# Performance work log

Hardware: AMD Instinct MI355X
Metric: run time of the kernel (lower is better)

## Reference

```python
import jax, jax.numpy as jnp
import numpy as np

BATCH, SEQ, DIN, FILTERS, KSIZE = 64, 512, 256, 256, 3

def setup_inputs() -> dict:
    key = jax.random.key(0)
    ks = jax.random.split(key, 5)
    s_u = 1.0 / np.sqrt(DIN)
    return {
        "x": jax.random.normal(ks[0], (BATCH, SEQ, DIN), dtype=jnp.float32),
        "z": jax.random.normal(ks[1], (BATCH, DIN), dtype=jnp.float32),
        "U": jax.random.normal(ks[2], (DIN, DIN), dtype=jnp.float32) * s_u,
        "V": jax.random.normal(ks[3], (DIN, KSIZE * FILTERS), dtype=jnp.float32) * s_u,
        "B_w": jax.random.normal(ks[4], (DIN, KSIZE * FILTERS), dtype=jnp.float32) * s_u,
        "b": jnp.zeros((FILTERS,), dtype=jnp.float32),
        "kernel_size": KSIZE,
    }

def reference(x, z, U, V, B_w, b, kernel_size):
    Bn, L, din = x.shape
    K = int(kernel_size)
    F = V.shape[1] // K
    # per-sample dynamic kernel: (U * sigmoid(z)) @ V + B
    zf = jax.nn.sigmoid(z)                                  # (B, din)
    f = jnp.einsum('de,be,ef->bdf', U, zf, V) + B_w[None]    # (B, din, K*F)
    f = f.reshape(Bn, din, K, F).transpose(0, 2, 1, 3)       # (B, K, din, F)
    # 'same' padding, stride 1
    pad_l, pad_r = (K - 1) // 2, K // 2
    xp = jnp.pad(x, ((0, 0), (pad_l, pad_r), (0, 0)))        # (B, L+K-1, din)
    patches = jnp.stack([xp[:, i:i + L] for i in range(K)], axis=2)  # (B, L, K, din)
    out = jnp.einsum('blkd,bkdf->blf', patches, f) + b       # (B, L, F)
    return jax.nn.relu(out)
```

## Files before the change

kernel.cpp:

```cpp
#include <hip/hip_runtime.h>
#include <math.h>

#define BATCH 64
#define SEQL  512
#define DIN   256
#define NF    256
#define KS    3
#define KF    (KS * NF)

#define XCH 512
#define KC  (KS * XCH)
#define PROWS 130
#define PLD   128
#define PSZ   (PROWS * PLD)

typedef __attribute__((ext_vector_type(8))) short short8;
typedef __attribute__((ext_vector_type(4))) float floatx4;
typedef __attribute__((ext_vector_type(16))) float floatx16;
typedef __attribute__((ext_vector_type(8))) unsigned short ushort8v;

static __device__ __forceinline__ unsigned short f2bf(float f) {
    unsigned int u = __float_as_uint(f);
    return (unsigned short)((u + 0x7FFF + ((u >> 16) & 1)) >> 16);
}

static __device__ __forceinline__ void gl_lds16(const void* g, void* l) {
    __builtin_amdgcn_global_load_lds(
        (const __attribute__((address_space(1))) unsigned int*)g,
        (__attribute__((address_space(3))) unsigned int*)l, 16, 0, 0);
}

__global__ __launch_bounds__(256) void pack_kernel(
    const float* __restrict__ U, const float* __restrict__ V,
    const float* __restrict__ Bw,
    unsigned short* __restrict__ WcT, unsigned short* __restrict__ UT)
{
    const int blk = blockIdx.x;
    const int t   = threadIdx.x;
    __shared__ unsigned short tile[64][64 + 2];

    if (blk < 96) {
        const int f0 = (blk & 3) * 64, c0 = (blk >> 2) * 64;
        const int fl = t & 63, cb = t >> 6;
        #pragma unroll
        for (int it = 0; it < 16; ++it) {
            const int cl = cb + it * 4;
            const int c  = c0 + cl;
            const int k  = c >> 9, ch = c & (XCH - 1);
            const float v = (ch < DIN) ? Bw[(size_t)ch * KF + k * NF + f0 + fl]
                                       : V[(size_t)(ch - DIN) * KF + k * NF + f0 + fl];
            tile[cl][fl] = f2bf(v);
        }
        __syncthreads();
        const int cl2 = t & 63, fb = t >> 6;
        #pragma unroll
        for (int it = 0; it < 16; ++it) {
            const int fl2 = fb + it * 4;
            WcT[(size_t)(f0 + fl2) * KC + c0 + cl2] = tile[cl2][fl2];
        }
    } else {
        const int bb = blk - 96;
        const int e0 = (bb & 3) * 64, d0 = (bb >> 2) * 64;
        const int el = t & 63, db = t >> 6;
        #pragma unroll
        for (int it = 0; it < 16; ++it) {
            const int dl = db + it * 4;
            tile[dl][el] = f2bf(U[(size_t)(d0 + dl) * DIN + e0 + el]);
        }
        __syncthreads();
        const int dl2 = t & 63, eb = t >> 6;
        #pragma unroll
        for (int it = 0; it < 16; ++it) {
            const int el2 = eb + it * 4;
            UT[(size_t)(e0 + el2) * DIN + d0 + dl2] = tile[dl2][el2];
        }
    }
}

__global__ __launch_bounds__(512, 2) void fused_kernel(
    const float* __restrict__ x, const float* __restrict__ z,
    const unsigned short* __restrict__ UT,
    const unsigned short* __restrict__ WcT,
    const float* __restrict__ bias, float* __restrict__ out)
{
    __shared__ __align__(16) unsigned short lds[4 * PSZ];

    const int tid  = threadIdx.x;
    const int lane = tid & 63;
    const int wave = tid >> 6;
    const int quad = lane >> 4, l16 = lane & 15;
    const int l32  = lane & 31, hi  = lane >> 5;
    const int r8   = lane >> 3, ud8 = lane & 7;

    const int bid   = blockIdx.x;
    const int b     = bid >> 2;
    const int lbase = (bid & 3) * 128;

    const int wr = wave >> 2, wc = wave & 3;

    floatx16 acc[2][2] = {};

    auto convBuf = [&](int r) -> unsigned short* {
        return (r < 12) ? (lds + 2 * PSZ + ((r & 1) ? 16384 : 0))
                        : (lds + ((r & 1) ? PSZ : 0));
    };
    auto stageB = [&](int r) {
        unsigned short* buf = convBuf(r);
        const int g = r / 6, k = (r / 2) % 3, hh = r & 1;
        const unsigned short* gW = WcT + (size_t)k * XCH + g * 128 + hh * 64;
        #pragma unroll
        for (int c = 0; c < 4; ++c) {
            const int rr = wave * 32 + c * 8 + r8;
            gl_lds16(gW + (size_t)rr * KC + ((ud8 ^ (rr & 7)) << 3),
                     buf + (size_t)(wave * 32 + c * 8) * 64);
        }
    };
    auto convRegion = [&](int r) {
        const unsigned short* buf = convBuf(r);
        const int g = r / 6, k = (r / 2) % 3, hh = r & 1;
        const unsigned short* P = lds + (size_t)g * PSZ;
        __builtin_amdgcn_s_setprio(1);
        #pragma unroll
        for (int ks = 0; ks < 4; ++ks) {
            short8 af[2], bf[2];
            const int uwa = hh * 8 + ks * 2 + hi;
            #pragma unroll
            for (int i = 0; i < 2; ++i) {
                const int m = wr * 64 + i * 32 + l32 + k;
                af[i] = *(const short8*)&P[m * PLD + ((uwa ^ (m & 15)) << 3)];
            }
            const int uwb = ks * 2 + hi;
            #pragma unroll
            for (int j = 0; j < 2; ++j) {
                const int n = wc * 64 + j * 32 + l32;
                bf[j] = *(const short8*)&buf[n * 64 + ((uwb ^ (n & 7)) << 3)];
            }
            #pragma unroll
            for (int i = 0; i < 2; ++i)
                #pragma unroll
                for (int j = 0; j < 2; ++j)
                    acc[i][j] = __builtin_amdgcn_mfma_f32_32x32x16_bf16(
                        af[i], bf[j], acc[i][j], 0, 0, 0);
        }
        __builtin_amdgcn_s_setprio(0);
    };

    #pragma unroll
    for (int p = 0; p < 2; ++p) {
        unsigned short* P = lds + (size_t)p * PSZ;
        #pragma unroll
        for (int it = 0; it < 5; ++it) {
            const int idx = tid + it * 512;
            if (idx < PROWS * 16) {
                const int row = idx >> 4, u = idx & 15;
                const int l = lbase - 1 + row;
                ushort8v h = {};
                if (l >= 0 && l < SEQL) {
                    const float* xp = x + ((size_t)b * SEQL + l) * DIN + p * 128 + u * 8;
                    const float4 v0 = *(const float4*)xp;
                    const float4 v1 = *(const float4*)(xp + 4);
                    h[0] = f2bf(v0.x); h[1] = f2bf(v0.y);
                    h[2] = f2bf(v0.z); h[3] = f2bf(v0.w);
                    h[4] = f2bf(v1.x); h[5] = f2bf(v1.y);
                    h[6] = f2bf(v1.z); h[7] = f2bf(v1.w);
                }
                *(ushort8v*)&P[row * PLD + ((u ^ (row & 15)) << 3)] = h;
            }
        }
    }

    stageB(0);
    __syncthreads();
    #pragma unroll 1
    for (int r = 0; r < 12; ++r) {
        if (r < 11) stageB(r + 1);
        convRegion(r);
        __syncthreads();
    }

    {
        floatx4 accY[2][9] = {};
        auto utBuf = [&](int kk) -> unsigned short* {
            return lds + 2 * PSZ + ((kk & 1) ? 16384 : 0);
        };
        auto stageU = [&](int kk) {
            unsigned short* buf = utBuf(kk);
            const unsigned short* gU = UT + (size_t)kk * 64;
            #pragma unroll
            for (int c = 0; c < 4; ++c) {
                const int rr = wave * 32 + c * 8 + r8;
                gl_lds16(gU + (size_t)rr * DIN + ((ud8 ^ (rr & 7)) << 3),
                         buf + (size_t)(wave * 32 + c * 8) * 64);
            }
        };
        stageU(0);
        __syncthreads();
        #pragma unroll 1
        for (int kk = 0; kk < 4; ++kk) {
            if (kk < 3) stageU(kk + 1);
            const unsigned short* buf = utBuf(kk);
            const unsigned short* P = lds + (size_t)(kk >> 1) * PSZ;
            const int dh = kk & 1;
            __builtin_amdgcn_s_setprio(1);
            #pragma unroll
            for (int ks = 0; ks < 2; ++ks) {
                short8 bfv[2];
                #pragma unroll
                for (int eh = 0; eh < 2; ++eh) {
                    const int n = eh * 128 + wave * 16 + l16;
                    bfv[eh] = *(const short8*)
                        &buf[n * 64 + (((ks * 4 + quad) ^ (n & 7)) << 3)];
                }
                #pragma unroll
                for (int i = 0; i < 9; ++i) {
                    const int row = i * 16 + l16;
                    const short8 afv = *(const short8*)
                        &P[row * PLD + (((dh * 8 + ks * 4 + quad) ^ (row & 15)) << 3)];
                    #pragma unroll
                    for (int eh = 0; eh < 2; ++eh)
                        accY[eh][i] = __builtin_amdgcn_mfma_f32_16x16x32_bf16(
                            afv, bfv[eh], accY[eh][i], 0, 0, 0);
                }
            }
            __builtin_amdgcn_s_setprio(0);
            __syncthreads();
        }
        #pragma unroll
        for (int eh = 0; eh < 2; ++eh) {
            const int ecol = wave * 16 + l16;
            const float zf = 1.0f /
                (1.0f + expf(-z[(size_t)b * DIN + eh * 128 + ecol]));
            unsigned short* PY = lds + (size_t)(2 + eh) * PSZ;
            const int u16e = ecol >> 3;
            #pragma unroll
            for (int i = 0; i < 9; ++i)
                #pragma unroll
                for (int rr2 = 0; rr2 < 4; ++rr2) {
                    const int row = i * 16 + quad * 4 + rr2;
                    if (row < PROWS)
                        PY[row * PLD + ((u16e ^ (row & 15)) << 3) + (ecol & 7)] =
                            f2bf(accY[eh][i][rr2] * zf);
                }
        }
    }

    stageB(12);
    __syncthreads();
    #pragma unroll 1
    for (int r = 12; r < 24; ++r) {
        if (r < 23) stageB(r + 1);
        convRegion(r);
        __syncthreads();
    }

    #pragma unroll
    for (int j = 0; j < 2; ++j) {
        const int f  = wc * 64 + j * 32 + l32;
        const float bv = bias[f];
        #pragma unroll
        for (int i = 0; i < 2; ++i) {
            #pragma unroll
            for (int reg = 0; reg < 16; ++reg) {
                const int rowl = wr * 64 + i * 32 + (reg & 3) + 8 * (reg >> 2) + 4 * hi;
                const float v = acc[i][j][reg] + bv;
                out[((size_t)b * SEQL + lbase + rowl) * NF + f] = fmaxf(v, 0.0f);
            }
        }
    }
}

extern "C" void kernel_launch(void* const* d_in, const int* in_sizes, int n_in,
                              void* d_out, int out_size, void* d_ws, size_t ws_size,
                              hipStream_t stream) {
    const float* x    = (const float*)d_in[0];
    const float* z    = (const float*)d_in[1];
    const float* U    = (const float*)d_in[2];
    const float* V    = (const float*)d_in[3];
    const float* Bw   = (const float*)d_in[4];
    const float* bias = (const float*)d_in[5];

    unsigned short* WcT = (unsigned short*)d_ws;
    unsigned short* UT  = WcT + (size_t)NF * KC;
    float* out = (float*)d_out;

    pack_kernel<<<dim3(112), 256, 0, stream>>>(U, V, Bw, WcT, UT);
    fused_kernel<<<dim3(256), 512, 0, stream>>>(x, z, UT, WcT, bias, out);
}
```

Measured before the change: 128.4 us.

## Split conv K dimension across wave pairs with larger tiles and LDS reduction

New measurement: 134.0 us. 4.4% more time.

```diff
diff --git a/kernel.cpp b/kernel.cpp
--- a/kernel.cpp
+++ b/kernel.cpp
@@ -18,6 +18,7 @@
 typedef __attribute__((ext_vector_type(4))) float floatx4;
 typedef __attribute__((ext_vector_type(16))) float floatx16;
 typedef __attribute__((ext_vector_type(8))) unsigned short ushort8v;
+typedef __attribute__((ext_vector_type(4))) unsigned short ushort4v;
 
 static __device__ __forceinline__ unsigned short f2bf(float f) {
     unsigned int u = __float_as_uint(f);
@@ -96,9 +97,12 @@
     const int b     = bid >> 2;
     const int lbase = (bid & 3) * 128;
 
-    const int wr = wave >> 2, wc = wave & 3;
-
-    floatx16 acc[2][2] = {};
+    const int tile4 = wave >> 1;
+    const int wr2   = tile4 >> 1;
+    const int wc2   = tile4 & 1;
+    const int kh    = wave & 1;
+
+    floatx16 acc2[2][4] = {};
 
     auto convBuf = [&](int r) -> unsigned short* {
         return (r < 12) ? (lds + 2 * PSZ + ((r & 1) ? 16384 : 0))
@@ -121,26 +125,27 @@
         const unsigned short* P = lds + (size_t)g * PSZ;
         __builtin_amdgcn_s_setprio(1);
         #pragma unroll
-        for (int ks = 0; ks < 4; ++ks) {
-            short8 af[2], bf[2];
+        for (int ks2 = 0; ks2 < 2; ++ks2) {
+            const int ks = kh * 2 + ks2;
+            short8 af[2], bf[4];
             const int uwa = hh * 8 + ks * 2 + hi;
             #pragma unroll
             for (int i = 0; i < 2; ++i) {
-                const int m = wr * 64 + i * 32 + l32 + k;
+                const int m = wr2 * 64 + i * 32 + l32 + k;
                 af[i] = *(const short8*)&P[m * PLD + ((uwa ^ (m & 15)) << 3)];
             }
             const int uwb = ks * 2 + hi;
             #pragma unroll
-            for (int j = 0; j < 2; ++j) {
-                const int n = wc * 64 + j * 32 + l32;
+            for (int j = 0; j < 4; ++j) {
+                const int n = wc2 * 128 + j * 32 + l32;
                 bf[j] = *(const short8*)&buf[n * 64 + ((uwb ^ (n & 7)) << 3)];
             }
             #pragma unroll
             for (int i = 0; i < 2; ++i)
                 #pragma unroll
-                for (int j = 0; j < 2; ++j)
-                    acc[i][j] = __builtin_amdgcn_mfma_f32_32x32x16_bf16(
-                        af[i], bf[j], acc[i][j], 0, 0, 0);
+                for (int j = 0; j < 4; ++j)
+                    acc2[i][j] = __builtin_amdgcn_mfma_f32_32x32x16_bf16(
+                        af[i], bf[j], acc2[i][j], 0, 0, 0);
         }
         __builtin_amdgcn_s_setprio(0);
     };
@@ -204,22 +209,22 @@
             __builtin_amdgcn_s_setprio(1);
             #pragma unroll
             for (int ks = 0; ks < 2; ++ks) {
-                short8 bfv[2];
+                short8 uf[2];
                 #pragma unroll
                 for (int eh = 0; eh < 2; ++eh) {
                     const int n = eh * 128 + wave * 16 + l16;
-                    bfv[eh] = *(const short8*)
+                    uf[eh] = *(const short8*)
                         &buf[n * 64 + (((ks * 4 + quad) ^ (n & 7)) << 3)];
                 }
                 #pragma unroll
                 for (int i = 0; i < 9; ++i) {
                     const int row = i * 16 + l16;
-                    const short8 afv = *(const short8*)
+                    const short8 xf = *(const short8*)
                         &P[row * PLD + (((dh * 8 + ks * 4 + quad) ^ (row & 15)) << 3)];
                     #pragma unroll
                     for (int eh = 0; eh < 2; ++eh)
                         accY[eh][i] = __builtin_amdgcn_mfma_f32_16x16x32_bf16(
-                            afv, bfv[eh], accY[eh][i], 0, 0, 0);
+                            uf[eh], xf, accY[eh][i], 0, 0, 0);
                 }
             }
             __builtin_amdgcn_s_setprio(0);
@@ -227,20 +232,25 @@
         }
         #pragma unroll
         for (int eh = 0; eh < 2; ++eh) {
-            const int ecol = wave * 16 + l16;
-            const float zf = 1.0f /
-                (1.0f + expf(-z[(size_t)b * DIN + eh * 128 + ecol]));
             unsigned short* PY = lds + (size_t)(2 + eh) * PSZ;
-            const int u16e = ecol >> 3;
-            #pragma unroll
-            for (int i = 0; i < 9; ++i)
-                #pragma unroll
-                for (int rr2 = 0; rr2 < 4; ++rr2) {
-                    const int row = i * 16 + quad * 4 + rr2;
-                    if (row < PROWS)
-                        PY[row * PLD + ((u16e ^ (row & 15)) << 3) + (ecol & 7)] =
-                            f2bf(accY[eh][i][rr2] * zf);
-                }
+            const int c0 = wave * 16 + quad * 4;
+            float zf[4];
+            #pragma unroll
+            for (int r2 = 0; r2 < 4; ++r2)
+                zf[r2] = 1.0f /
+                    (1.0f + expf(-z[(size_t)b * DIN + eh * 128 + c0 + r2]));
+            const int u = c0 >> 3;
+            #pragma unroll
+            for (int i = 0; i < 9; ++i) {
+                const int xrow = i * 16 + l16;
+                if (xrow < PROWS) {
+                    ushort4v h;
+                    #pragma unroll
+                    for (int r2 = 0; r2 < 4; ++r2)
+                        h[r2] = f2bf(accY[eh][i][r2] * zf[r2]);
+                    *(ushort4v*)&PY[xrow * PLD + ((u ^ (xrow & 15)) << 3) + (c0 & 7)] = h;
+                }
+            }
         }
     }
 
@@ -253,17 +263,55 @@
         __syncthreads();
     }
 
-    #pragma unroll
-    for (int j = 0; j < 2; ++j) {
-        const int f  = wc * 64 + j * 32 + l32;
-        const float bv = bias[f];
-        #pragma unroll
-        for (int i = 0; i < 2; ++i) {
-            #pragma unroll
-            for (int reg = 0; reg < 16; ++reg) {
-                const int rowl = wr * 64 + i * 32 + (reg & 3) + 8 * (reg >> 2) + 4 * hi;
-                const float v = acc[i][j][reg] + bv;
-                out[((size_t)b * SEQL + lbase + rowl) * NF + f] = fmaxf(v, 0.0f);
+    {
+        float* fbuf = (float*)lds;
+        float* wA = fbuf + (size_t)tile4 * 8192 + (size_t)kh * 4096;
+        #pragma unroll
+        for (int jp = 0; jp < 2; ++jp) {
+            if (jp != kh) {
+                #pragma unroll
+                for (int i = 0; i < 2; ++i)
+                    #pragma unroll
+                    for (int jj = 0; jj < 2; ++jj)
+                        #pragma unroll
+                        for (int q = 0; q < 4; ++q) {
+                            floatx4 v;
+                            #pragma unroll
+                            for (int c2 = 0; c2 < 4; ++c2)
+                                v[c2] = acc2[i][jp * 2 + jj][q * 4 + c2];
+                            *(floatx4*)&wA[(size_t)(((i * 2 + jj) * 4 + q) * 256
+                                                    + lane * 4)] = v;
+                        }
+            }
+        }
+        __syncthreads();
+        const float* rA = fbuf + (size_t)tile4 * 8192 + (size_t)(1 - kh) * 4096;
+        #pragma unroll
+        for (int jp = 0; jp < 2; ++jp) {
+            if (jp == kh) {
+                #pragma unroll
+                for (int jj = 0; jj < 2; ++jj) {
+                    const int f  = wc2 * 128 + (jp * 2 + jj) * 32 + l32;
+                    const float bv = bias[f];
+                    #pragma unroll
+                    for (int i = 0; i < 2; ++i) {
+                        #pragma unroll
+                        for (int q = 0; q < 4; ++q) {
+                            const floatx4 v = *(const floatx4*)
+                                &rA[(size_t)(((i * 2 + jj) * 4 + q) * 256 + lane * 4)];
+                            #pragma unroll
+                            for (int c2 = 0; c2 < 4; ++c2) {
+                                const int reg  = q * 4 + c2;
+                                const int rowl = wr2 * 64 + i * 32 +
+                                                 (reg & 3) + 8 * (reg >> 2) + 4 * hi;
+                                const float val =
+                                    acc2[i][jp * 2 + jj][reg] + v[c2] + bv;
+                                out[((size_t)b * SEQL + lbase + rowl) * NF + f] =
+                                    fmaxf(val, 0.0f);
+                            }
+                        }
+                    }
+                }
             }
         }
     }
```

## Halve fused conv tile to 64 rows with 256-thread blocks and 512-block grid

Applied to the files above, without the earlier changes.

New measurement: 136.9 us. +6.7%, slower.

```diff
diff --git a/kernel.cpp b/kernel.cpp
--- a/kernel.cpp
+++ b/kernel.cpp
@@ -10,14 +10,15 @@
 
 #define XCH 512
 #define KC  (KS * XCH)
-#define PROWS 130
-#define PLD   128
-#define PSZ   (PROWS * PLD)
+#define PR2 66
+#define PLD 128
+#define P0SZ (PR2 * PLD)
 
 typedef __attribute__((ext_vector_type(8))) short short8;
 typedef __attribute__((ext_vector_type(4))) float floatx4;
 typedef __attribute__((ext_vector_type(16))) float floatx16;
 typedef __attribute__((ext_vector_type(8))) unsigned short ushort8v;
+typedef __attribute__((ext_vector_type(4))) unsigned short ushort4v;
 
 static __device__ __forceinline__ unsigned short f2bf(float f) {
     unsigned int u = __float_as_uint(f);
@@ -77,86 +78,143 @@
     }
 }
 
-__global__ __launch_bounds__(512, 2) void fused_kernel(
+__global__ __launch_bounds__(256, 2) void fused_kernel(
     const float* __restrict__ x, const float* __restrict__ z,
     const unsigned short* __restrict__ UT,
     const unsigned short* __restrict__ WcT,
     const float* __restrict__ bias, float* __restrict__ out)
 {
-    __shared__ __align__(16) unsigned short lds[4 * PSZ];
+    __shared__ __align__(16) unsigned short lds[2 * P0SZ + 2 * 8192];
+    unsigned short* P0 = lds;
+    unsigned short* P1 = lds + P0SZ;
+    unsigned short* Bs = lds + 2 * P0SZ;
 
     const int tid  = threadIdx.x;
     const int lane = tid & 63;
     const int wave = tid >> 6;
     const int quad = lane >> 4, l16 = lane & 15;
     const int l32  = lane & 31, hi  = lane >> 5;
-    const int r8   = lane >> 3, ud8 = lane & 7;
-
-    const int bid   = blockIdx.x;
-    const int b     = bid >> 2;
-    const int lbase = (bid & 3) * 128;
-
-    const int wr = wave >> 2, wc = wave & 3;
-
-    floatx16 acc[2][2] = {};
-
-    auto convBuf = [&](int r) -> unsigned short* {
-        return (r < 12) ? (lds + 2 * PSZ + ((r & 1) ? 16384 : 0))
-                        : (lds + ((r & 1) ? PSZ : 0));
+    const int r4   = lane >> 2, ud4 = lane & 3;
+
+    const int bid = blockIdx.x;
+    const int b   = bid >> 3;
+    const int l0  = (bid & 7) * 64;
+
+    floatx16 acc2[2][2] = {};
+    floatx4  accY[4][5] = {};
+
+    auto stage32 = [&](const unsigned short* gbase, size_t rs,
+                       unsigned short* buf) {
+        #pragma unroll
+        for (int c = 0; c < 4; ++c) {
+            const int rr = wave * 64 + c * 16 + r4;
+            gl_lds16(gbase + (size_t)rr * rs + ((ud4 ^ (rr & 3)) << 3),
+                     buf + (size_t)(wave * 64 + c * 16) * 32);
+        }
     };
     auto stageB = [&](int r) {
-        unsigned short* buf = convBuf(r);
-        const int g = r / 6, k = (r / 2) % 3, hh = r & 1;
-        const unsigned short* gW = WcT + (size_t)k * XCH + g * 128 + hh * 64;
-        #pragma unroll
-        for (int c = 0; c < 4; ++c) {
-            const int rr = wave * 32 + c * 8 + r8;
-            gl_lds16(gW + (size_t)rr * KC + ((ud8 ^ (rr & 7)) << 3),
-                     buf + (size_t)(wave * 32 + c * 8) * 64);
-        }
-    };
+        const int g = r / 12, k = (r / 4) % 3, hq = r & 3;
+        stage32(WcT + (size_t)k * XCH + g * 128 + hq * 32, KC,
+                Bs + (size_t)(r & 1) * 8192);
+    };
+    auto stageU = [&](int kk) {
+        stage32(UT + (size_t)kk * 32, DIN, Bs + (size_t)(kk & 1) * 8192);
+    };
+
     auto convRegion = [&](int r) {
-        const unsigned short* buf = convBuf(r);
-        const int g = r / 6, k = (r / 2) % 3, hh = r & 1;
-        const unsigned short* P = lds + (size_t)g * PSZ;
+        const unsigned short* buf = Bs + (size_t)(r & 1) * 8192;
+        const int g = r / 12, k = (r / 4) % 3, hq = r & 3;
+        const unsigned short* P = (g & 1) ? P1 : P0;
         __builtin_amdgcn_s_setprio(1);
         #pragma unroll
-        for (int ks = 0; ks < 4; ++ks) {
+        for (int ks = 0; ks < 2; ++ks) {
             short8 af[2], bf[2];
-            const int uwa = hh * 8 + ks * 2 + hi;
+            const int ua = hq * 4 + ks * 2 + hi;
             #pragma unroll
             for (int i = 0; i < 2; ++i) {
-                const int m = wr * 64 + i * 32 + l32 + k;
-                af[i] = *(const short8*)&P[m * PLD + ((uwa ^ (m & 15)) << 3)];
-            }
-            const int uwb = ks * 2 + hi;
+                const int m = i * 32 + l32 + k;
+                af[i] = *(const short8*)&P[m * PLD + ((ua ^ (m & 15)) << 3)];
+            }
+            const int ub = ks * 2 + hi;
             #pragma unroll
             for (int j = 0; j < 2; ++j) {
-                const int n = wc * 64 + j * 32 + l32;
-                bf[j] = *(const short8*)&buf[n * 64 + ((uwb ^ (n & 7)) << 3)];
+                const int n = wave * 64 + j * 32 + l32;
+                bf[j] = *(const short8*)&buf[n * 32 + ((ub ^ (n & 3)) << 3)];
             }
             #pragma unroll
             for (int i = 0; i < 2; ++i)
                 #pragma unroll
                 for (int j = 0; j < 2; ++j)
-                    acc[i][j] = __builtin_amdgcn_mfma_f32_32x32x16_bf16(
-                        af[i], bf[j], acc[i][j], 0, 0, 0);
+                    acc2[i][j] = __builtin_amdgcn_mfma_f32_32x32x16_bf16(
+                        af[i], bf[j], acc2[i][j], 0, 0, 0);
         }
         __builtin_amdgcn_s_setprio(0);
+    };
+
+    auto gChunk = [&](int kk) {
+        const unsigned short* buf = Bs + (size_t)(kk & 1) * 8192;
+        const unsigned short* P = (kk >= 4) ? P1 : P0;
+        const int ux = (kk & 3) * 4 + quad;
+        __builtin_amdgcn_s_setprio(1);
+        short8 uf[4];
+        #pragma unroll
+        for (int q = 0; q < 4; ++q) {
+            const int n = q * 64 + wave * 16 + l16;
+            uf[q] = *(const short8*)&buf[n * 32 + ((quad ^ (n & 3)) << 3)];
+        }
+        #pragma unroll
+        for (int i = 0; i < 5; ++i) {
+            const int row = i * 16 + l16;
+            const short8 xf = *(const short8*)
+                &P[row * PLD + ((ux ^ (row & 15)) << 3)];
+            #pragma unroll
+            for (int q = 0; q < 4; ++q)
+                accY[q][i] = __builtin_amdgcn_mfma_f32_16x16x32_bf16(
+                    uf[q], xf, accY[q][i], 0, 0, 0);
+        }
+        __builtin_amdgcn_s_setprio(0);
+    };
+
+    auto yEpi = [&](int eh) {
+        unsigned short* PY = eh ? P1 : P0;
+        #pragma unroll
+        for (int q2 = 0; q2 < 2; ++q2) {
+            const int q  = eh * 2 + q2;
+            const int e0 = (q * 4 + wave) * 16 + quad * 4;
+            const int c0 = e0 & 127;
+            float zf[4];
+            #pragma unroll
+            for (int r2 = 0; r2 < 4; ++r2)
+                zf[r2] = 1.0f / (1.0f + expf(-z[(size_t)b * DIN + e0 + r2]));
+            const int u = c0 >> 3;
+            #pragma unroll
+            for (int i = 0; i < 5; ++i) {
+                const int xrow = i * 16 + l16;
+                if (xrow < PR2) {
+                    ushort4v h;
+                    #pragma unroll
+                    for (int r2 = 0; r2 < 4; ++r2)
+                        h[r2] = f2bf(accY[q][i][r2] * zf[r2]);
+                    *(ushort4v*)&PY[xrow * PLD + ((u ^ (xrow & 15)) << 3) +
+                                    (c0 & 7)] = h;
+                }
+            }
+        }
     };
 
     #pragma unroll
     for (int p = 0; p < 2; ++p) {
-        unsigned short* P = lds + (size_t)p * PSZ;
+        unsigned short* P = p ? P1 : P0;
         #pragma unroll
         for (int it = 0; it < 5; ++it) {
-            const int idx = tid + it * 512;
-            if (idx < PROWS * 16) {
+            const int idx = tid + it * 256;
+            if (idx < PR2 * 16) {
                 const int row = idx >> 4, u = idx & 15;
-                const int l = lbase - 1 + row;
+                const int l = l0 - 1 + row;
                 ushort8v h = {};
                 if (l >= 0 && l < SEQL) {
-                    const float* xp = x + ((size_t)b * SEQL + l) * DIN + p * 128 + u * 8;
+                    const float* xp =
+                        x + ((size_t)b * SEQL + l) * DIN + p * 128 + u * 8;
                     const float4 v0 = *(const float4*)xp;
                     const float4 v1 = *(const float4*)(xp + 4);
                     h[0] = f2bf(v0.x); h[1] = f2bf(v0.y);
@@ -169,101 +227,41 @@
         }
     }
 
-    stageB(0);
+    stageU(0);
     __syncthreads();
     #pragma unroll 1
-    for (int r = 0; r < 12; ++r) {
-        if (r < 11) stageB(r + 1);
-        convRegion(r);
-        __syncthreads();
-    }
-
-    {
-        floatx4 accY[2][9] = {};
-        auto utBuf = [&](int kk) -> unsigned short* {
-            return lds + 2 * PSZ + ((kk & 1) ? 16384 : 0);
-        };
-        auto stageU = [&](int kk) {
-            unsigned short* buf = utBuf(kk);
-            const unsigned short* gU = UT + (size_t)kk * 64;
-            #pragma unroll
-            for (int c = 0; c < 4; ++c) {
-                const int rr = wave * 32 + c * 8 + r8;
-                gl_lds16(gU + (size_t)rr * DIN + ((ud8 ^ (rr & 7)) << 3),
-                         buf + (size_t)(wave * 32 + c * 8) * 64);
-            }
-        };
-        stageU(0);
-        __syncthreads();
-        #pragma unroll 1
-        for (int kk = 0; kk < 4; ++kk) {
-            if (kk < 3) stageU(kk + 1);
-            const unsigned short* buf = utBuf(kk);
-            const unsigned short* P = lds + (size_t)(kk >> 1) * PSZ;
-            const int dh = kk & 1;
-            __builtin_amdgcn_s_setprio(1);
-            #pragma unroll
-            for (int ks = 0; ks < 2; ++ks) {
-                short8 bfv[2];
-                #pragma unroll
-                for (int eh = 0; eh < 2; ++eh) {
-                    const int n = eh * 128 + wave * 16 + l16;
-                    bfv[eh] = *(const short8*)
-                        &buf[n * 64 + (((ks * 4 + quad) ^ (n & 7)) << 3)];
-                }
-                #pragma unroll
-                for (int i = 0; i < 9; ++i) {
-                    const int row = i * 16 + l16;
-                    const short8 afv = *(const short8*)
-                        &P[row * PLD + (((dh * 8 + ks * 4 + quad) ^ (row & 15)) << 3)];
-                    #pragma unroll
-                    for (int eh = 0; eh < 2; ++eh)
-                        accY[eh][i] = __builtin_amdgcn_mfma_f32_16x16x32_bf16(
-                            afv, bfv[eh], accY[eh][i], 0, 0, 0);
-                }
-            }
-            __builtin_amdgcn_s_setprio(0);
-            __syncthreads();
-        }
-        #pragma unroll
-        for (int eh = 0; eh < 2; ++eh) {
-            const int ecol = wave * 16 + l16;
-            const float zf = 1.0f /
-                (1.0f + expf(-z[(size_t)b * DIN + eh * 128 + ecol]));
-            unsigned short* PY = lds + (size_t)(2 + eh) * PSZ;
-            const int u16e = ecol >> 3;
-            #pragma unroll
-            for (int i = 0; i < 9; ++i)
-                #pragma unroll
-                for (int rr2 = 0; rr2 < 4; ++rr2) {
-                    const int row = i * 16 + quad * 4 + rr2;
-                    if (row < PROWS)
-                        PY[row * PLD + ((u16e ^ (row & 15)) << 3) + (ecol & 7)] =
-                            f2bf(accY[eh][i][rr2] * zf);
-                }
-        }
-    }
-
-    stageB(12);
-    __syncthreads();
-    #pragma unroll 1
-    for (int r = 12; r < 24; ++r) {
-        if (r < 23) stageB(r + 1);
+    for (int kk = 0; kk < 8; ++kk) {
+        if (kk < 7) stageU(kk + 1); else stageB(0);
+        gChunk(kk);
+        __syncthreads();
+    }
+
+    #pragma unroll 1
+    for (int r = 0; r < 12; ++r) { stageB(r + 1); convRegion(r); __syncthreads(); }
+    yEpi(0);
+
+    #pragma unroll 1
+    for (int r = 12; r < 24; ++r) { stageB(r + 1); convRegion(r); __syncthreads(); }
+    yEpi(1);
+
+    #pragma unroll 1
+    for (int r = 24; r < 48; ++r) {
+        if (r < 47) stageB(r + 1);
         convRegion(r);
         __syncthreads();
     }
 
     #pragma unroll
     for (int j = 0; j < 2; ++j) {
-        const int f  = wc * 64 + j * 32 + l32;
+        const int f  = wave * 64 + j * 32 + l32;
         const float bv = bias[f];
         #pragma unroll
         for (int i = 0; i < 2; ++i) {
             #pragma unroll
             for (int reg = 0; reg < 16; ++reg) {
-                const int rowl = wr * 64 + i * 32 + (reg & 3) + 8 * (reg >> 2) + 4 * hi;
-                const float v = acc[i][j][reg] + bv;
-                out[((size_t)b * SEQL + lbase + rowl) * NF + f] = fmaxf(v, 0.0f);
+                const int rowl = i * 32 + (reg & 3) + 8 * (reg >> 2) + 4 * hi;
+                const float v = acc2[i][j][reg] + bv;
+                out[((size_t)b * SEQL + l0 + rowl) * NF + f] = fmaxf(v, 0.0f);
             }
         }
     }
@@ -284,5 +282,5 @@
     float* out = (float*)d_out;
 
     pack_kernel<<<dim3(112), 256, 0, stream>>>(U, V, Bw, WcT, UT);
-    fused_kernel<<<dim3(256), 512, 0, stream>>>(x, z, UT, WcT, bias, out);
-}
+    fused_kernel<<<dim3(512), 256, 0, stream>>>(x, z, UT, WcT, bias, out);
+}
```

## Deepen weight staging to a four-slot ring with fine-grained vmcnt waits

Applied to the files above, without the earlier changes.

After: 131.3 us. +2.3%, slower.

```diff
diff --git a/kernel.cpp b/kernel.cpp
--- a/kernel.cpp
+++ b/kernel.cpp
@@ -13,11 +13,13 @@
 #define PROWS 130
 #define PLD   128
 #define PSZ   (PROWS * PLD)
+#define SLOT  8192
 
 typedef __attribute__((ext_vector_type(8))) short short8;
 typedef __attribute__((ext_vector_type(4))) float floatx4;
 typedef __attribute__((ext_vector_type(16))) float floatx16;
 typedef __attribute__((ext_vector_type(8))) unsigned short ushort8v;
+typedef __attribute__((ext_vector_type(4))) unsigned short ushort4v;
 
 static __device__ __forceinline__ unsigned short f2bf(float f) {
     unsigned int u = __float_as_uint(f);
@@ -29,6 +31,18 @@
         (const __attribute__((address_space(1))) unsigned int*)g,
         (__attribute__((address_space(3))) unsigned int*)l, 16, 0, 0);
 }
+
+#define PIPE_WAIT(rem)                                                       \
+    do {                                                                     \
+        if ((rem) >= 2)                                                      \
+            asm volatile("s_waitcnt vmcnt(4) lgkmcnt(0)" ::: "memory");      \
+        else if ((rem) == 1)                                                 \
+            asm volatile("s_waitcnt vmcnt(2) lgkmcnt(0)" ::: "memory");      \
+        else                                                                 \
+            asm volatile("s_waitcnt vmcnt(0) lgkmcnt(0)" ::: "memory");      \
+        __builtin_amdgcn_s_barrier();                                        \
+        __builtin_amdgcn_sched_barrier(0);                                   \
+    } while (0)
 
 __global__ __launch_bounds__(256) void pack_kernel(
     const float* __restrict__ U, const float* __restrict__ V,
@@ -90,60 +104,73 @@
     const int wave = tid >> 6;
     const int quad = lane >> 4, l16 = lane & 15;
     const int l32  = lane & 31, hi  = lane >> 5;
-    const int r8   = lane >> 3, ud8 = lane & 7;
 
     const int bid   = blockIdx.x;
     const int b     = bid >> 2;
     const int lbase = (bid & 3) * 128;
 
-    const int wr = wave >> 2, wc = wave & 3;
-
-    floatx16 acc[2][2] = {};
-
-    auto convBuf = [&](int r) -> unsigned short* {
-        return (r < 12) ? (lds + 2 * PSZ + ((r & 1) ? 16384 : 0))
-                        : (lds + ((r & 1) ? PSZ : 0));
+    const int wr = wave >> 2, wcv = wave & 3;
+
+    floatx16 acc2[2][2] = {};
+
+    unsigned short* RA = lds + 2 * PSZ;
+    unsigned short* RB = lds;
+
+    auto stagePair = [&](const unsigned short* gbase, size_t rs,
+                         unsigned short* buf) {
+        #pragma unroll
+        for (int c = 0; c < 2; ++c) {
+            const int group = wave * 2 + c;
+            const int lr    = group * 8 + (lane >> 3);
+            const int gr    = lr * 2 + ((lane >> 2) & 1);
+            const int chunk = (lane & 3) ^ (lr & 3);
+            gl_lds16(gbase + (size_t)gr * rs + chunk * 8,
+                     buf + (size_t)group * 512);
+        }
     };
     auto stageB = [&](int r) {
-        unsigned short* buf = convBuf(r);
-        const int g = r / 6, k = (r / 2) % 3, hh = r & 1;
-        const unsigned short* gW = WcT + (size_t)k * XCH + g * 128 + hh * 64;
-        #pragma unroll
-        for (int c = 0; c < 4; ++c) {
-            const int rr = wave * 32 + c * 8 + r8;
-            gl_lds16(gW + (size_t)rr * KC + ((ud8 ^ (rr & 7)) << 3),
-                     buf + (size_t)(wave * 32 + c * 8) * 64);
-        }
+        const int g = r / 12, k = (r >> 2) % 3, cq = r & 3;
+        stagePair(WcT + (size_t)k * XCH + g * 128 + cq * 32, KC,
+                  ((r < 24) ? RA : RB) + (size_t)(r & 3) * SLOT);
     };
+    auto stageU = [&](int kk) {
+        stagePair(UT + (size_t)kk * 32, DIN, RA + (size_t)(kk & 3) * SLOT);
+    };
+
     auto convRegion = [&](int r) {
-        const unsigned short* buf = convBuf(r);
-        const int g = r / 6, k = (r / 2) % 3, hh = r & 1;
+        const unsigned short* buf =
+            ((r < 24) ? RA : RB) + (size_t)(r & 3) * SLOT;
+        const int g = r / 12, k = (r >> 2) % 3, cq = r & 3;
         const unsigned short* P = lds + (size_t)g * PSZ;
         __builtin_amdgcn_s_setprio(1);
         #pragma unroll
-        for (int ks = 0; ks < 4; ++ks) {
+        for (int ks = 0; ks < 2; ++ks) {
             short8 af[2], bf[2];
-            const int uwa = hh * 8 + ks * 2 + hi;
+            const int ua = cq * 4 + ks * 2 + hi;
             #pragma unroll
             for (int i = 0; i < 2; ++i) {
                 const int m = wr * 64 + i * 32 + l32 + k;
-                af[i] = *(const short8*)&P[m * PLD + ((uwa ^ (m & 15)) << 3)];
-            }
-            const int uwb = ks * 2 + hi;
+                af[i] = *(const short8*)&P[m * PLD + ((ua ^ (m & 15)) << 3)];
+            }
+            const int ci = ks * 2 + hi;
             #pragma unroll
             for (int j = 0; j < 2; ++j) {
-                const int n = wc * 64 + j * 32 + l32;
-                bf[j] = *(const short8*)&buf[n * 64 + ((uwb ^ (n & 7)) << 3)];
+                const int n = wcv * 64 + j * 32 + l32;
+                bf[j] = *(const short8*)
+                    &buf[(n >> 1) * 64 +
+                         ((((n & 1) * 4) + (ci ^ ((n >> 1) & 3))) << 3)];
             }
             #pragma unroll
             for (int i = 0; i < 2; ++i)
                 #pragma unroll
                 for (int j = 0; j < 2; ++j)
-                    acc[i][j] = __builtin_amdgcn_mfma_f32_32x32x16_bf16(
-                        af[i], bf[j], acc[i][j], 0, 0, 0);
+                    acc2[i][j] = __builtin_amdgcn_mfma_f32_32x32x16_bf16(
+                        af[i], bf[j], acc2[i][j], 0, 0, 0);
         }
         __builtin_amdgcn_s_setprio(0);
     };
+
+    stageB(0); stageB(1); stageB(2);
 
     #pragma unroll
     for (int p = 0; p < 2; ++p) {
@@ -156,7 +183,8 @@
                 const int l = lbase - 1 + row;
                 ushort8v h = {};
                 if (l >= 0 && l < SEQL) {
-                    const float* xp = x + ((size_t)b * SEQL + l) * DIN + p * 128 + u * 8;
+                    const float* xp =
+                        x + ((size_t)b * SEQL + l) * DIN + p * 128 + u * 8;
                     const float4 v0 = *(const float4*)xp;
                     const float4 v1 = *(const float4*)(xp + 4);
                     h[0] = f2bf(v0.x); h[1] = f2bf(v0.y);
@@ -169,100 +197,92 @@
         }
     }
 
-    stageB(0);
-    __syncthreads();
     #pragma unroll 1
-    for (int r = 0; r < 12; ++r) {
-        if (r < 11) stageB(r + 1);
+    for (int r = 0; r < 24; ++r) {
+        PIPE_WAIT(23 - r);
+        if (r + 3 < 24) stageB(r + 3);
         convRegion(r);
-        __syncthreads();
     }
 
     {
         floatx4 accY[2][9] = {};
-        auto utBuf = [&](int kk) -> unsigned short* {
-            return lds + 2 * PSZ + ((kk & 1) ? 16384 : 0);
-        };
-        auto stageU = [&](int kk) {
-            unsigned short* buf = utBuf(kk);
-            const unsigned short* gU = UT + (size_t)kk * 64;
-            #pragma unroll
-            for (int c = 0; c < 4; ++c) {
-                const int rr = wave * 32 + c * 8 + r8;
-                gl_lds16(gU + (size_t)rr * DIN + ((ud8 ^ (rr & 7)) << 3),
-                         buf + (size_t)(wave * 32 + c * 8) * 64);
-            }
-        };
-        stageU(0);
-        __syncthreads();
+        stageU(0); stageU(1); stageU(2);
         #pragma unroll 1
-        for (int kk = 0; kk < 4; ++kk) {
-            if (kk < 3) stageU(kk + 1);
-            const unsigned short* buf = utBuf(kk);
-            const unsigned short* P = lds + (size_t)(kk >> 1) * PSZ;
-            const int dh = kk & 1;
+        for (int kk = 0; kk < 8; ++kk) {
+            PIPE_WAIT(7 - kk);
+            if (kk + 3 < 8) stageU(kk + 3);
+            const unsigned short* buf = RA + (size_t)(kk & 3) * SLOT;
+            const unsigned short* P = lds + (size_t)((kk >= 4) ? 1 : 0) * PSZ;
+            const int ub = (kk & 3) * 4 + quad;
             __builtin_amdgcn_s_setprio(1);
-            #pragma unroll
-            for (int ks = 0; ks < 2; ++ks) {
-                short8 bfv[2];
+            short8 uf[2];
+            #pragma unroll
+            for (int eh = 0; eh < 2; ++eh) {
+                const int n = eh * 128 + wave * 16 + l16;
+                uf[eh] = *(const short8*)
+                    &buf[(n >> 1) * 64 +
+                         ((((n & 1) * 4) + (quad ^ ((n >> 1) & 3))) << 3)];
+            }
+            #pragma unroll
+            for (int i = 0; i < 9; ++i) {
+                const int row = i * 16 + l16;
+                const short8 xf = *(const short8*)
+                    &P[row * PLD + ((ub ^ (row & 15)) << 3)];
                 #pragma unroll
-                for (int eh = 0; eh < 2; ++eh) {
-                    const int n = eh * 128 + wave * 16 + l16;
-                    bfv[eh] = *(const short8*)
-                        &buf[n * 64 + (((ks * 4 + quad) ^ (n & 7)) << 3)];
+                for (int eh = 0; eh < 2; ++eh)
+                    accY[eh][i] = __builtin_amdgcn_mfma_f32_16x16x32_bf16(
+                        uf[eh], xf, accY[eh][i], 0, 0, 0);
+            }
+            __builtin_amdgcn_s_setprio(0);
+        }
+        asm volatile("s_waitcnt lgkmcnt(0)" ::: "memory");
+        __builtin_amdgcn_s_barrier();
+        __builtin_amdgcn_sched_barrier(0);
+
+        #pragma unroll
+        for (int eh = 0; eh < 2; ++eh) {
+            unsigned short* PY = lds + (size_t)(2 + eh) * PSZ;
+            const int c0 = wave * 16 + quad * 4;
+            float zf[4];
+            #pragma unroll
+            for (int r2 = 0; r2 < 4; ++r2)
+                zf[r2] = 1.0f /
+                    (1.0f + expf(-z[(size_t)b * DIN + eh * 128 + c0 + r2]));
+            const int u = c0 >> 3;
+            #pragma unroll
+            for (int i = 0; i < 9; ++i) {
+                const int xrow = i * 16 + l16;
+                if (xrow < PROWS) {
+                    ushort4v h;
+                    #pragma unroll
+                    for (int r2 = 0; r2 < 4; ++r2)
+                        h[r2] = f2bf(accY[eh][i][r2] * zf[r2]);
+                    *(ushort4v*)&PY[xrow * PLD + ((u ^ (xrow & 15)) << 3) +
+                                    (c0 & 7)] = h;
                 }
-                #pragma unroll
-                for (int i = 0; i < 9; ++i) {
-                    const int row = i * 16 + l16;
-                    const short8 afv = *(const short8*)
-                        &P[row * PLD + (((dh * 8 + ks * 4 + quad) ^ (row & 15)) << 3)];
-                    #pragma unroll
-                    for (int eh = 0; eh < 2; ++eh)
-                        accY[eh][i] = __builtin_amdgcn_mfma_f32_16x16x32_bf16(
-                            afv, bfv[eh], accY[eh][i], 0, 0, 0);
-                }
-            }
-            __builtin_amdgcn_s_setprio(0);
-            __syncthreads();
-        }
-        #pragma unroll
-        for (int eh = 0; eh < 2; ++eh) {
-            const int ecol = wave * 16 + l16;
-            const float zf = 1.0f /
-                (1.0f + expf(-z[(size_t)b * DIN + eh * 128 + ecol]));
-            unsigned short* PY = lds + (size_t)(2 + eh) * PSZ;
-            const int u16e = ecol >> 3;
-            #pragma unroll
-            for (int i = 0; i < 9; ++i)
-                #pragma unroll
-                for (int rr2 = 0; rr2 < 4; ++rr2) {
-                    const int row = i * 16 + quad * 4 + rr2;
-                    if (row < PROWS)
-                        PY[row * PLD + ((u16e ^ (row & 15)) << 3) + (ecol & 7)] =
-                            f2bf(accY[eh][i][rr2] * zf);
-                }
-        }
-    }
-
-    stageB(12);
-    __syncthreads();
+            }
+        }
+    }
+
+    stageB(24); stageB(25); stageB(26);
     #pragma unroll 1
-    for (int r = 12; r < 24; ++r) {
-        if (r < 23) stageB(r + 1);
+    for (int r = 24; r < 48; ++r) {
+        PIPE_WAIT(47 - r);
+        if (r + 3 < 48) stageB(r + 3);
         convRegion(r);
-        __syncthreads();
     }
 
     #pragma unroll
     for (int j = 0; j < 2; ++j) {
-        const int f  = wc * 64 + j * 32 + l32;
+        const int f  = wcv * 64 + j * 32 + l32;
         const float bv = bias[f];
         #pragma unroll
         for (int i = 0; i < 2; ++i) {
             #pragma unroll
             for (int reg = 0; reg < 16; ++reg) {
-                const int rowl = wr * 64 + i * 32 + (reg & 3) + 8 * (reg >> 2) + 4 * hi;
-                const float v = acc[i][j][reg] + bv;
+                const int rowl = wr * 64 + i * 32 +
+                                 (reg & 3) + 8 * (reg >> 2) + 4 * hi;
+                const float v = acc2[i][j][reg] + bv;
                 out[((size_t)b * SEQL + lbase + rowl) * NF + f] = fmaxf(v, 0.0f);
             }
         }
```
